# Kernel tuning notes

Measured on AMD Instinct MI355X. Metric: run time of the kernel, lower is better.

Reference implementation:

```python
import jax, jax.numpy as jnp
import numpy as np

DIM = 256
HEADS = 8
WS = 8          # window_size[0]
N = WS * WS     # tokens per window
B = 2048        # number of windows (batch * windows_per_image)


def _rel_pos_indices(ws):
    # Reproduces: grid of (i,j) positions flattened, pairwise diff, shifted, flattened index
    pos = np.arange(ws)
    gy, gx = np.meshgrid(pos, pos, indexing='ij')
    grid = np.stack([gy.ravel(), gx.ravel()], axis=-1)          # (ws*ws, 2)
    rel = grid[:, None, :] - grid[None, :, :] + (ws - 1)        # (n, n, 2)
    idx = rel[..., 0] * (2 * ws - 1) + rel[..., 1]              # (n, n)
    return jnp.asarray(idx, dtype=jnp.int32)


def setup_inputs() -> dict:
    key = jax.random.key(0)
    ks = jax.random.split(key, 6)
    return {
        'x': jax.random.normal(ks[0], (B, N, DIM), dtype=jnp.float32),
        'qkv_w': jax.random.normal(ks[1], (3 * DIM, DIM), dtype=jnp.float32) * 0.02,
        'qkv_b': jax.random.normal(ks[2], (3 * DIM,), dtype=jnp.float32) * 0.02,
        'proj_w': jax.random.normal(ks[3], (DIM, DIM), dtype=jnp.float32) * 0.02,
        'proj_b': jax.random.normal(ks[4], (DIM,), dtype=jnp.float32) * 0.02,
        'bias_table': jax.random.normal(ks[5], ((2 * WS - 1) ** 2, HEADS), dtype=jnp.float32) * 0.02,
        'rel_pos_indices': _rel_pos_indices(WS),
    }


def reference(x, qkv_w, qkv_b, proj_w, proj_b, bias_table, rel_pos_indices):
    b, n, c = x.shape
    head_dim = c // HEADS
    scale = head_dim ** (-0.5)

    qkv = x @ qkv_w.T + qkv_b                                   # [b, n, 3c]
    q, k, v = jnp.split(qkv, 3, axis=-1)
    # b n (h d) -> b h n d
    to_heads = lambda t: t.reshape(b, n, HEADS, head_dim).transpose(0, 2, 1, 3)
    q, k, v = to_heads(q) * scale, to_heads(k), to_heads(v)

    # relative position bias: [n, n, h] -> [h, n, n]
    bias = bias_table[rel_pos_indices].transpose(2, 0, 1)

    attn = jnp.einsum('bhnd,bhmd->bhnm', q, k) + bias           # [b, h, n, n]
    attn = jax.nn.softmax(attn, axis=-1)
    out = jnp.einsum('bhnm,bhmd->bhnd', attn, v)                # [b, h, n, d]
    out = out.transpose(0, 2, 1, 3).reshape(b, n, c)
    out = out @ proj_w.T + proj_b
    return (out, attn)
```

## Files before the change

kernel.cpp:

```cpp
#include <hip/hip_runtime.h>

typedef __bf16 bf16;
typedef __attribute__((ext_vector_type(8))) __bf16 bf16x8;
typedef __attribute__((ext_vector_type(4))) __bf16 bf16x4;
typedef __attribute__((ext_vector_type(4))) float f32x4;

#define MFMA16(A, Bf, Cf) __builtin_amdgcn_mfma_f32_16x16x32_bf16((A), (Bf), (Cf), 0, 0, 0)

namespace {
constexpr int kB = 2048;
constexpr float kScale = 0.17677669529663687f;
constexpr size_t kOut0 = (size_t)kB * 64 * 256;
constexpr size_t kWqkvOff = 0;
constexpr size_t kWprojOff = 393216;
constexpr size_t kBiasOff = 524288;
}


__global__ void prep_kernel(const float* __restrict__ qkv_w,
                            const float* __restrict__ proj_w,
                            const float* __restrict__ bias_table,
                            const int* __restrict__ rel_idx,
                            bf16* __restrict__ qkv_wb,
                            bf16* __restrict__ proj_wb,
                            float* __restrict__ biasf) {
  int t = blockIdx.x * 256 + threadIdx.x;
  if (t < 196608) {
    qkv_wb[t] = (bf16)qkv_w[t];
  } else if (t < 262144) {
    int u = t - 196608;
    proj_wb[u] = (bf16)proj_w[u];
  } else if (t < 294912) {
    int u = t - 262144;
    int h = u >> 12;
    int v = u & 4095;
    int wv = v >> 10;
    int ct = (v >> 8) & 3;
    int lane = (v >> 2) & 63;
    int r = v & 3;
    int row = wv * 16 + (lane >> 4) * 4 + r;
    int col = ct * 16 + (lane & 15);
    biasf[u] = bias_table[rel_idx[row * 64 + col] * 8 + h];
  }
}

__launch_bounds__(256, 3)
__global__ void qkv_kernel(const float* __restrict__ x,
                           const float* __restrict__ qkv_b,
                           const bf16* __restrict__ qkv_wb,
                           float* __restrict__ out,
                           float* __restrict__ attn_out) {
  __shared__ __align__(16) bf16 xb[64 * 264];
  const int t = threadIdx.x;
  const int wave = t >> 6;
  const int lane = t & 63;
  const int l16 = lane & 15;
  const int quad = lane >> 4;
  const int b = blockIdx.x;
  const int wr = wave >> 1;
  const int wc = wave & 1;
  const f32x4 fz = {0.f, 0.f, 0.f, 0.f};

  {
    const f32x4* xv = (const f32x4*)(x + (size_t)b * 16384);
#pragma unroll
    for (int i = 0; i < 16; ++i) {
      int g4 = i * 256 + t;
      f32x4 v = xv[g4];
      int row = g4 >> 6;
      int c4 = (g4 & 63) << 2;
      bf16x4 w;
      w.x = (bf16)v.x; w.y = (bf16)v.y; w.z = (bf16)v.z; w.w = (bf16)v.w;
      *(bf16x4*)&xb[row * 264 + c4] = w;
    }
  }
  __syncthreads();

  bf16x8 afr[2][8];
#pragma unroll
  for (int rt = 0; rt < 2; ++rt)
#pragma unroll
    for (int kt = 0; kt < 8; ++kt)
      afr[rt][kt] =
          *(const bf16x8*)&xb[(wr * 32 + rt * 16 + l16) * 264 + kt * 32 + quad * 8];

  bf16* qkst = (bf16*)(attn_out + (size_t)b * 32768);
  bf16* vst  = (bf16*)(out + (size_t)b * 16384);

#pragma unroll 2
  for (int nt = 0; nt < 24; ++nt) {
    int col16 = wc * 384 + nt * 16;
    const bf16* wp = qkv_wb + (col16 + l16) * 256 + quad * 8;
    bf16x8 bfr[8];
#pragma unroll
    for (int kt = 0; kt < 8; ++kt) bfr[kt] = *(const bf16x8*)&wp[kt * 32];
    f32x4 a0 = fz, a1 = fz;
#pragma unroll
    for (int kt = 0; kt < 8; ++kt) {
      a0 = MFMA16(afr[0][kt], bfr[kt], a0);
      a1 = MFMA16(afr[1][kt], bfr[kt], a1);
    }
    int col = col16 + l16;
    float qb = qkv_b[col];
    float sc = (col16 < 256) ? kScale : 1.0f;
#pragma unroll
    for (int rt = 0; rt < 2; ++rt) {
      f32x4 a = rt ? a1 : a0;
#pragma unroll
      for (int r = 0; r < 4; ++r) {
        int row = wr * 32 + rt * 16 + quad * 4 + r;
        float val = (a[r] + qb) * sc;
        if (col16 < 512) qkst[row * 512 + col] = (bf16)val;
        else             vst[row * 256 + (col - 512)] = (bf16)val;
      }
    }
  }
}

__launch_bounds__(256, 3)
__global__ void attn2_kernel(const float* __restrict__ biasf,
                             float* __restrict__ out,
                             float* __restrict__ attn_out) {
  __shared__ __align__(16) bf16 kl[64 * 264];
  __shared__ __align__(16) bf16 vT[2][32 * 72];
  __shared__ __align__(16) bf16 Pb[64 * 72];

  const int t = threadIdx.x;
  const int wave = t >> 6;
  const int lane = t & 63;
  const int l16 = lane & 15;
  const int quad = lane >> 4;
  const int b = blockIdx.x;
  const int mrow = wave * 16 + l16;
  const f32x4 fz = {0.f, 0.f, 0.f, 0.f};

  const bf16* qkst = (const bf16*)(attn_out + (size_t)b * 32768);
  const bf16* vst  = (const bf16*)(out + (size_t)b * 16384);
  bf16* ost = (bf16*)(out + (size_t)b * 16384) + 16384;

  bf16x8 qf[8];
#pragma unroll
  for (int h = 0; h < 8; ++h)
    qf[h] = *(const bf16x8*)&qkst[mrow * 512 + h * 32 + quad * 8];

  {
    int row = t >> 2, part = t & 3;
#pragma unroll
    for (int j = 0; j < 8; ++j) {
      bf16x8 v = *(const bf16x8*)&qkst[row * 512 + 256 + part * 64 + j * 8];
      *(bf16x8*)&kl[row * 264 + part * 64 + j * 8] = v;
    }
  }
  {
    int tok = t >> 2, dp = t & 3;
    bf16x8 v = *(const bf16x8*)&vst[tok * 256 + dp * 8];
#pragma unroll
    for (int j = 0; j < 8; ++j) vT[0][(dp * 8 + j) * 72 + tok] = v[j];
  }
  __syncthreads();

#pragma unroll
  for (int h = 0; h < 8; ++h) {
    int tok = t >> 2, dp = t & 3;
    bf16x8 vnext;
    if (h < 7) vnext = *(const bf16x8*)&vst[tok * 256 + (h + 1) * 32 + dp * 8];

    f32x4 bfrag[4];
    const f32x4* bp4 = (const f32x4*)(biasf + h * 4096 + wave * 1024);
#pragma unroll
    for (int ct = 0; ct < 4; ++ct) bfrag[ct] = bp4[ct * 64 + lane];

    f32x4 s[4];
#pragma unroll
    for (int ct = 0; ct < 4; ++ct) {
      bf16x8 bS = *(const bf16x8*)&kl[(ct * 16 + l16) * 264 + h * 32 + quad * 8];
      s[ct] = MFMA16(qf[h], bS, bfrag[ct]);
    }

#pragma unroll
    for (int r = 0; r < 4; ++r) {
      float m = fmaxf(fmaxf(s[0][r], s[1][r]), fmaxf(s[2][r], s[3][r]));
#pragma unroll
      for (int off = 8; off; off >>= 1) m = fmaxf(m, __shfl_xor(m, off));
      float e0 = __expf(s[0][r] - m);
      float e1 = __expf(s[1][r] - m);
      float e2 = __expf(s[2][r] - m);
      float e3 = __expf(s[3][r] - m);
      float sum = (e0 + e1) + (e2 + e3);
#pragma unroll
      for (int off = 8; off; off >>= 1) sum += __shfl_xor(sum, off);
      float is = 1.0f / sum;
      s[0][r] = e0 * is; s[1][r] = e1 * is; s[2][r] = e2 * is; s[3][r] = e3 * is;
    }

    float* ao = attn_out + ((size_t)(b * 8 + h) << 12);
#pragma unroll
    for (int ct = 0; ct < 4; ++ct)
#pragma unroll
      for (int r = 0; r < 4; ++r) {
        int i = wave * 16 + quad * 4 + r;
        int j = ct * 16 + l16;
        float pv = s[ct][r];
        ao[i * 64 + j] = pv;
        Pb[i * 72 + j] = (bf16)pv;
      }

    f32x4 o[2];
    o[0] = fz; o[1] = fz;
#pragma unroll
    for (int ks = 0; ks < 2; ++ks) {
      bf16x8 aP = *(const bf16x8*)&Pb[mrow * 72 + ks * 32 + quad * 8];
#pragma unroll
      for (int nt = 0; nt < 2; ++nt) {
        bf16x8 bV = *(const bf16x8*)&vT[h & 1][(nt * 16 + l16) * 72 + ks * 32 + quad * 8];
        o[nt] = MFMA16(aP, bV, o[nt]);
      }
    }

#pragma unroll
    for (int nt = 0; nt < 2; ++nt)
#pragma unroll
      for (int r = 0; r < 4; ++r)
        ost[(wave * 16 + quad * 4 + r) * 256 + h * 32 + nt * 16 + l16] =
            (bf16)o[nt][r];

    if (h < 7) {
#pragma unroll
      for (int j = 0; j < 8; ++j)
        vT[(h + 1) & 1][(dp * 8 + j) * 72 + tok] = vnext[j];
    }
    __syncthreads();
  }
}

__launch_bounds__(256, 3)
__global__ void proj_kernel(const float* __restrict__ proj_b,
                            const bf16* __restrict__ proj_wb,
                            float* __restrict__ out) {
  const int t = threadIdx.x;
  const int wave = t >> 6;
  const int lane = t & 63;
  const int l16 = lane & 15;
  const int quad = lane >> 4;
  const int b = blockIdx.x;
  const int mrow = wave * 16 + l16;
  const f32x4 fz = {0.f, 0.f, 0.f, 0.f};

  const bf16* ost = (const bf16*)(out + (size_t)b * 16384) + 16384;
  bf16x8 oafr[8];
#pragma unroll
  for (int kt = 0; kt < 8; ++kt)
    oafr[kt] = *(const bf16x8*)&ost[mrow * 256 + kt * 32 + quad * 8];

  f32x4 acc[16];
#pragma unroll
  for (int i = 0; i < 16; ++i) acc[i] = fz;
#pragma unroll
  for (int nt = 0; nt < 16; ++nt) {
    const bf16* wp = proj_wb + (nt * 16 + l16) * 256 + quad * 8;
    bf16x8 bfr[8];
#pragma unroll
    for (int kt = 0; kt < 8; ++kt) bfr[kt] = *(const bf16x8*)&wp[kt * 32];
#pragma unroll
    for (int kt = 0; kt < 8; ++kt) acc[nt] = MFMA16(oafr[kt], bfr[kt], acc[nt]);
  }
  __syncthreads();

  float* op = out + (size_t)b * 16384;
#pragma unroll
  for (int nt = 0; nt < 16; ++nt) {
    float pb = proj_b[nt * 16 + l16];
#pragma unroll
    for (int r = 0; r < 4; ++r)
      op[(wave * 16 + quad * 4 + r) * 256 + nt * 16 + l16] = acc[nt][r] + pb;
  }
}

extern "C" void kernel_launch(void* const* d_in, const int* in_sizes, int n_in,
                              void* d_out, int out_size, void* d_ws, size_t ws_size,
                              hipStream_t stream) {
  const float* x          = (const float*)d_in[0];
  const float* qkv_w      = (const float*)d_in[1];
  const float* qkv_b      = (const float*)d_in[2];
  const float* proj_w     = (const float*)d_in[3];
  const float* proj_b     = (const float*)d_in[4];
  const float* bias_table = (const float*)d_in[5];
  const int*   rel_idx    = (const int*)d_in[6];

  bf16*  qkv_wb = (bf16*)((char*)d_ws + kWqkvOff);
  bf16*  proj_wb = (bf16*)((char*)d_ws + kWprojOff);
  float* biasf  = (float*)((char*)d_ws + kBiasOff);

  float* out      = (float*)d_out;
  float* attn_out = out + kOut0;

  prep_kernel<<<1152, 256, 0, stream>>>(qkv_w, proj_w, bias_table, rel_idx,
                                        qkv_wb, proj_wb, biasf);
  qkv_kernel<<<kB, 256, 0, stream>>>(x, qkv_b, qkv_wb, out, attn_out);
  attn2_kernel<<<kB, 256, 0, stream>>>(biasf, out, attn_out);
  proj_kernel<<<kB, 256, 0, stream>>>(proj_b, proj_wb, out);
}
```

Measured before the change: 929.5 us.

## Pre-convert x to bf16 and retile QKV GEMM into 128x128 LDS-staged tiles

The x-to-bf16 conversion moves into the prep kernel, which writes bf16 x into spare space in the attention output buffer. The QKV projection becomes a conventional tiled GEMM: each block computes a 128x128 output tile over two windows, staging A and B K-slices through LDS. This gives more reuse of weights and activations per block than the per-window kernel, which reloaded all weights from global memory for every window. In exchange it adds an extra global round-trip for bf16 x, more grid blocks, and a non-pipelined load/sync loop.

```diff
diff --git a/kernel.cpp b/kernel.cpp
--- a/kernel.cpp
+++ b/kernel.cpp
@@ -17,13 +17,15 @@
 }
 
 
-__global__ void prep_kernel(const float* __restrict__ qkv_w,
+__global__ void prep_kernel(const float* __restrict__ x,
+                            const float* __restrict__ qkv_w,
                             const float* __restrict__ proj_w,
                             const float* __restrict__ bias_table,
                             const int* __restrict__ rel_idx,
                             bf16* __restrict__ qkv_wb,
                             bf16* __restrict__ proj_wb,
-                            float* __restrict__ biasf) {
+                            float* __restrict__ biasf,
+                            float* __restrict__ attn_out) {
   int t = blockIdx.x * 256 + threadIdx.x;
   if (t < 196608) {
     qkv_wb[t] = (bf16)qkv_w[t];
@@ -41,79 +43,104 @@
     int row = wv * 16 + (lane >> 4) * 4 + r;
     int col = ct * 16 + (lane & 15);
     biasf[u] = bias_table[rel_idx[row * 64 + col] * 8 + h];
+  } else if (t < 294912 + 4194304) {
+    int u = t - 294912;
+    size_t e = (size_t)u * 8;
+    int win = (int)(e >> 14);
+    int rem = (int)(e & 16383);
+    int lrow = rem >> 8;
+    int col = rem & 255;
+    const f32x4* xs = (const f32x4*)(x + e);
+    f32x4 v0 = xs[0], v1 = xs[1];
+    bf16x8 w;
+    w[0] = (bf16)v0.x; w[1] = (bf16)v0.y; w[2] = (bf16)v0.z; w[3] = (bf16)v0.w;
+    w[4] = (bf16)v1.x; w[5] = (bf16)v1.y; w[6] = (bf16)v1.z; w[7] = (bf16)v1.w;
+    bf16* xbf = (bf16*)((char*)attn_out + (size_t)win * 131072 + 65536);
+    *(bf16x8*)&xbf[lrow * 256 + col] = w;
   }
 }
 
 __launch_bounds__(256, 3)
-__global__ void qkv_kernel(const float* __restrict__ x,
-                           const float* __restrict__ qkv_b,
+__global__ void qkv_kernel(const float* __restrict__ qkv_b,
                            const bf16* __restrict__ qkv_wb,
                            float* __restrict__ out,
                            float* __restrict__ attn_out) {
-  __shared__ __align__(16) bf16 xb[64 * 264];
+  __shared__ __align__(16) bf16 As[128 * 40];
+  __shared__ __align__(16) bf16 Bs[128 * 40];
+
   const int t = threadIdx.x;
   const int wave = t >> 6;
   const int lane = t & 63;
   const int l16 = lane & 15;
   const int quad = lane >> 4;
-  const int b = blockIdx.x;
+  const int bid = blockIdx.x;
+  const int mt = bid / 6;
+  const int nt = bid % 6;
   const int wr = wave >> 1;
   const int wc = wave & 1;
   const f32x4 fz = {0.f, 0.f, 0.f, 0.f};
 
-  {
-    const f32x4* xv = (const f32x4*)(x + (size_t)b * 16384);
-#pragma unroll
-    for (int i = 0; i < 16; ++i) {
-      int g4 = i * 256 + t;
-      f32x4 v = xv[g4];
-      int row = g4 >> 6;
-      int c4 = (g4 & 63) << 2;
-      bf16x4 w;
-      w.x = (bf16)v.x; w.y = (bf16)v.y; w.z = (bf16)v.z; w.w = (bf16)v.w;
-      *(bf16x4*)&xb[row * 264 + c4] = w;
-    }
-  }
-  __syncthreads();
-
-  bf16x8 afr[2][8];
-#pragma unroll
-  for (int rt = 0; rt < 2; ++rt)
-#pragma unroll
-    for (int kt = 0; kt < 8; ++kt)
-      afr[rt][kt] =
-          *(const bf16x8*)&xb[(wr * 32 + rt * 16 + l16) * 264 + kt * 32 + quad * 8];
-
-  bf16* qkst = (bf16*)(attn_out + (size_t)b * 32768);
-  bf16* vst  = (bf16*)(out + (size_t)b * 16384);
-
-#pragma unroll 2
-  for (int nt = 0; nt < 24; ++nt) {
-    int col16 = wc * 384 + nt * 16;
-    const bf16* wp = qkv_wb + (col16 + l16) * 256 + quad * 8;
-    bf16x8 bfr[8];
-#pragma unroll
-    for (int kt = 0; kt < 8; ++kt) bfr[kt] = *(const bf16x8*)&wp[kt * 32];
-    f32x4 a0 = fz, a1 = fz;
-#pragma unroll
-    for (int kt = 0; kt < 8; ++kt) {
-      a0 = MFMA16(afr[0][kt], bfr[kt], a0);
-      a1 = MFMA16(afr[1][kt], bfr[kt], a1);
-    }
-    int col = col16 + l16;
-    float qb = qkv_b[col];
-    float sc = (col16 < 256) ? kScale : 1.0f;
-#pragma unroll
-    for (int rt = 0; rt < 2; ++rt) {
-      f32x4 a = rt ? a1 : a0;
-#pragma unroll
-      for (int r = 0; r < 4; ++r) {
-        int row = wr * 32 + rt * 16 + quad * 4 + r;
-        float val = (a[r] + qb) * sc;
-        if (col16 < 512) qkst[row * 512 + col] = (bf16)val;
-        else             vst[row * 256 + (col - 512)] = (bf16)val;
+  const int r0 = t >> 2;
+  const int s0 = t & 3;
+
+  const bf16* xA0 = (const bf16*)((char*)attn_out + (size_t)(2 * mt) * 131072 + 65536);
+  const bf16* xA1 = (const bf16*)((char*)attn_out + (size_t)(2 * mt + 1) * 131072 + 65536);
+  const bf16* wB  = qkv_wb + (size_t)(nt * 128) * 256;
+
+  f32x4 acc[4][4];
+#pragma unroll
+  for (int i = 0; i < 4; ++i)
+#pragma unroll
+    for (int j = 0; j < 4; ++j) acc[i][j] = fz;
+
+#pragma unroll 1
+  for (int ks = 0; ks < 8; ++ks) {
+    const int kc = ks * 32 + s0 * 8;
+    bf16x8 a0 = *(const bf16x8*)&xA0[r0 * 256 + kc];
+    bf16x8 a1 = *(const bf16x8*)&xA1[r0 * 256 + kc];
+    bf16x8 b0 = *(const bf16x8*)&wB[r0 * 256 + kc];
+    bf16x8 b1 = *(const bf16x8*)&wB[(64 + r0) * 256 + kc];
+    __syncthreads();
+    *(bf16x8*)&As[r0 * 40 + s0 * 8] = a0;
+    *(bf16x8*)&As[(64 + r0) * 40 + s0 * 8] = a1;
+    *(bf16x8*)&Bs[r0 * 40 + s0 * 8] = b0;
+    *(bf16x8*)&Bs[(64 + r0) * 40 + s0 * 8] = b1;
+    __syncthreads();
+    bf16x8 af[4], bf_[4];
+#pragma unroll
+    for (int mf = 0; mf < 4; ++mf)
+      af[mf] = *(const bf16x8*)&As[(wr * 64 + mf * 16 + l16) * 40 + quad * 8];
+#pragma unroll
+    for (int nf = 0; nf < 4; ++nf)
+      bf_[nf] = *(const bf16x8*)&Bs[(wc * 64 + nf * 16 + l16) * 40 + quad * 8];
+#pragma unroll
+    for (int mf = 0; mf < 4; ++mf)
+#pragma unroll
+      for (int nf = 0; nf < 4; ++nf)
+        acc[mf][nf] = MFMA16(af[mf], bf_[nf], acc[mf][nf]);
+  }
+
+#pragma unroll
+  for (int nf = 0; nf < 4; ++nf) {
+    const int gcol = nt * 128 + wc * 64 + nf * 16 + l16;
+    const float qb = qkv_b[gcol];
+    const float sc = (gcol < 256) ? kScale : 1.0f;
+#pragma unroll
+    for (int mf = 0; mf < 4; ++mf)
+#pragma unroll
+      for (int rr = 0; rr < 4; ++rr) {
+        const int grow = mt * 128 + wr * 64 + mf * 16 + quad * 4 + rr;
+        const int win = grow >> 6;
+        const int lrow = grow & 63;
+        const float val = (acc[mf][nf][rr] + qb) * sc;
+        if (gcol < 512) {
+          bf16* qkst = (bf16*)((char*)attn_out + (size_t)win * 131072);
+          qkst[lrow * 512 + gcol] = (bf16)val;
+        } else {
+          bf16* vst = (bf16*)((char*)out + (size_t)win * 65536);
+          vst[lrow * 256 + (gcol - 512)] = (bf16)val;
+        }
       }
-    }
   }
 }
 
@@ -294,9 +321,9 @@
   float* out      = (float*)d_out;
   float* attn_out = out + kOut0;
 
-  prep_kernel<<<1152, 256, 0, stream>>>(qkv_w, proj_w, bias_table, rel_idx,
-                                        qkv_wb, proj_wb, biasf);
-  qkv_kernel<<<kB, 256, 0, stream>>>(x, qkv_b, qkv_wb, out, attn_out);
+  prep_kernel<<<17536, 256, 0, stream>>>(x, qkv_w, proj_w, bias_table, rel_idx,
+                                         qkv_wb, proj_wb, biasf, attn_out);
+  qkv_kernel<<<6144, 256, 0, stream>>>(qkv_b, qkv_wb, out, attn_out);
   attn2_kernel<<<kB, 256, 0, stream>>>(biasf, out, attn_out);
   proj_kernel<<<kB, 256, 0, stream>>>(proj_b, proj_wb, out);
 }
```

New measurement: 871.9 us. -6.2%, faster.
